# Performance work log

Hardware: AMD Instinct MI355X
Metric: run time of the kernel (lower is better)

Reference implementation:

```python
import jax, jax.numpy as jnp
import numpy as np

K = 8            # regular-rep dim (C_8), reg_dim
R_BINS = 3       # num_radii
T_BINS = 16      # num_theta
G = R_BINS * T_BINS
RADIUS = 40.0    # radius_scale
DT = 1.0
CORR = 1.0 / 128.0
SHIFT = 0.2
TWO_PI = 2.0 * np.pi

# [m,n] -> (m-n) mod K, for circulant (group-equivariant) linear maps on the regular rep
_SIDX = (np.arange(K)[:, None] - np.arange(K)[None, :]) % K


def _basis(ab):
    # learnable equivariant intertwiner rho1 <-> regular: a*u_m + b*u_m_perp
    th = jnp.arange(K, dtype=jnp.float32) * (TWO_PI / K)
    U = jnp.stack([jnp.cos(th), jnp.sin(th)], -1)       # [K,2]
    Up = jnp.stack([-jnp.sin(th), jnp.cos(th)], -1)
    return ab[0] * U + ab[1] * Up


def lift_rho1_to_reg(v, ab):
    # v [...,c,2] -> [...,c,K]
    return jnp.einsum('...ca,ma->...cm', v, _basis(ab))


def proj_reg_to_rho1(x, ab):
    # x [...,c,K] -> [...,c,2]
    return jnp.einsum('...cm,ma->...ca', x, _basis(ab))


def equi_linear_reg(x, W):
    # x [...,ci,K], W [co,ci,K]; out[...,o,m] = sum_{i,s} W[o,i,s] x[...,i,(m-s)%K]
    Wc = W[:, :, _SIDX]                                  # [co,ci,m,n]
    return jnp.einsum('...in,oimn->...om', x, Wc)


def _full_kernel(W):
    # base W [co,ci,K,R,T] -> rotated stack [K(m),co,ci,K(n),G]
    s = T_BINS // K
    kern = jnp.stack([jnp.roll(jnp.roll(W, m, axis=2), m * s, axis=4) for m in range(K)], 0)
    return kern.reshape(K, W.shape[0], W.shape[1], K, G)


def pair_bin_weights(p, mask):
    # Dense pairwise continuous-conv weights: window * bilinear polar-grid interpolation,
    # normalized by the neighbor window sum. p [B,N,2], mask [B,N] -> [B,N,N,G]
    N = p.shape[1]
    rel = p[:, None, :, :] - p[:, :, None, :]            # rel[b,i,j] = p_j - p_i
    d = jnp.sqrt(jnp.sum(rel * rel, -1) + 1e-12) / RADIUS
    window = jnp.maximum(1.0 - d * d, 0.0) ** 3          # radius cutoff + window
    wb = window * mask[:, None, :]
    wb = wb / (jnp.sum(wb, -1, keepdims=True) + 1e-6)    # neighbor normalization
    rc = jnp.clip(d * R_BINS - 0.5, 0.0, R_BINS - 1.0)
    r0 = jnp.floor(rc); wr = rc - r0
    r0i = r0.astype(jnp.int32); r1i = jnp.minimum(r0i + 1, R_BINS - 1)
    eye = jnp.eye(N, dtype=bool)[None]                   # safe atan2 at self-pairs
    rx = jnp.where(eye, 1.0, rel[..., 0]); ry = jnp.where(eye, 0.0, rel[..., 1])
    tc = (jnp.arctan2(ry, rx) % TWO_PI) / TWO_PI * T_BINS
    t0 = jnp.floor(tc); wt = tc - t0
    t0i = t0.astype(jnp.int32) % T_BINS; t1i = (t0i + 1) % T_BINS
    gs = [r0i * T_BINS + t0i, r0i * T_BINS + t1i, r1i * T_BINS + t0i, r1i * T_BINS + t1i]
    ws = [(1 - wr) * (1 - wt), (1 - wr) * wt, wr * (1 - wt), wr * wt]
    Wsum = jnp.zeros(d.shape + (G,), jnp.float32)
    for g, w in zip(gs, ws):
        Wsum = Wsum + (w * wb)[..., None] * jax.nn.one_hot(g, G, dtype=jnp.float32)
    return Wsum


def cts_conv(Wsum, feats, Wk):
    # feats [B,N,ci,K] -> [B,N,co,K]
    F = jnp.einsum('bijg,bjcn->bigcn', Wsum, feats)      # bin neighbor features onto polar grid
    return jnp.einsum('bigcn,mocng->biom', F, _full_kernel(Wk))


def mag_act(x):
    mags = jnp.sum(x * x, -1, keepdims=True) + 1e-6
    return x / mags * jax.nn.relu(mags - SHIFT)


def setup_inputs() -> dict:
    key = jax.random.key(0)
    B, N, T = 2, 512, 7
    ks = jax.random.split(key, 20)
    s = 0.05
    return {
        'p0_enc': jax.random.uniform(ks[0], (B, N, T, 2), jnp.float32) * 100.0,
        'v0_enc': jax.random.normal(ks[1], (B, N, T, 2), jnp.float32),
        'p0': jax.random.uniform(ks[2], (B, N, 2), jnp.float32) * 100.0,
        'v0': jax.random.normal(ks[3], (B, N, 2), jnp.float32),
        'a': jax.random.normal(ks[4], (B, N, 2), jnp.float32) * 0.1,
        'fluid_mask': jnp.ones((B, N), jnp.float32),
        'lift_c0': jax.random.normal(ks[5], (2,), jnp.float32) * s,
        'Wc0': jax.random.normal(ks[6], (4, 16, K, R_BINS, T_BINS), jnp.float32) * s,
        'lift_d0': jax.random.normal(ks[7], (2,), jnp.float32) * s,
        'Wd0': jax.random.normal(ks[8], (4, 16, K), jnp.float32) * s,
        'Wc1': jax.random.normal(ks[9], (8, 8, K, R_BINS, T_BINS), jnp.float32) * s,
        'Wd1': jax.random.normal(ks[10], (8, 8, K), jnp.float32) * s,
        'Wc2': jax.random.normal(ks[11], (16, 8, K, R_BINS, T_BINS), jnp.float32) * s,
        'Wd2': jax.random.normal(ks[12], (16, 8, K), jnp.float32) * s,
        'Wc3': jax.random.normal(ks[13], (8, 16, K, R_BINS, T_BINS), jnp.float32) * s,
        'Wd3': jax.random.normal(ks[14], (8, 16, K), jnp.float32) * s,
        'Wc4': jax.random.normal(ks[15], (3, 8, K, R_BINS, T_BINS), jnp.float32) * s,
        'proj_c4': jax.random.normal(ks[16], (2,), jnp.float32) * s,
        'Wd4': jax.random.normal(ks[17], (3, 8, K), jnp.float32) * s,
        'proj_d4': jax.random.normal(ks[18], (2,), jnp.float32) * s,
    }


def reference(p0_enc, v0_enc, p0, v0, a, fluid_mask,
              lift_c0, Wc0, lift_d0, Wd0, Wc1, Wd1, Wc2, Wd2,
              Wc3, Wd3, Wc4, proj_c4, Wd4, proj_d4):
    feats = jnp.concatenate([v0_enc, p0_enc], -2)        # [B,N,14,2]
    v1 = v0 + DT * a
    p1 = p0 + DT * (v0 + v1) / 2.0
    fluid_feats = jnp.concatenate([v1[:, :, None, :], p1[:, :, None, :], feats], -2)  # [B,N,16,2]
    Wsum = pair_bin_weights(p1, fluid_mask)              # shared across all conv layers
    out_conv = cts_conv(Wsum, lift_rho1_to_reg(fluid_feats, lift_c0), Wc0)
    out_dense = equi_linear_reg(lift_rho1_to_reg(fluid_feats, lift_d0), Wd0)
    output = jnp.concatenate([out_conv, out_dense], -2)  # [B,N,8,K]
    for Wc, Wd, last in ((Wc1, Wd1, False), (Wc2, Wd2, False), (Wc3, Wd3, False), (Wc4, Wd4, True)):
        in_feats = mag_act(output)
        oc = cts_conv(Wsum, in_feats, Wc)
        od = equi_linear_reg(in_feats, Wd)
        if last:
            oc = proj_reg_to_rho1(oc, proj_c4)
            od = proj_reg_to_rho1(od, proj_d4)
        new = oc + od
        if new.shape[-2] == output.shape[-2] and new.shape[-1] == output.shape[-1]:
            new = new + output
        output = new
    pos_correction = CORR * output                       # [B,N,3,2]
    p_corr = p1 + pos_correction[..., 0, :]
    v_corr = (p_corr - p0) / DT
    m_matrix = pos_correction[..., 1:, :]                # [B,N,2,2]
    return p_corr, v_corr, m_matrix
```

## Files before the change

### kernel.cpp

```cpp
#include <hip/hip_runtime.h>

#define NPART 1024
#define NNB   512
#define EMAX  2048

__global__ void prep_kernel(const float* __restrict__ p0_enc, const float* __restrict__ v0_enc,
                            const float* __restrict__ p0, const float* __restrict__ v0,
                            const float* __restrict__ a, const float* __restrict__ liftc,
                            const float* __restrict__ liftd,
                            float* __restrict__ featsC, float* __restrict__ Fbuf,
                            float* __restrict__ p1out)
{
    int p = blockIdx.x;
    int t = threadIdx.x;
    int c = t >> 3, m = t & 7;
    float v0x = v0[p*2+0], v0y = v0[p*2+1];
    float ax  = a[p*2+0],  ay  = a[p*2+1];
    float p0x = p0[p*2+0], p0y = p0[p*2+1];
    float v1x = v0x + ax, v1y = v0y + ay;
    float p1x = p0x + 0.5f*(v0x + v1x), p1y = p0y + 0.5f*(v0y + v1y);
    float vx, vy;
    if (c == 0)      { vx = v1x; vy = v1y; }
    else if (c == 1) { vx = p1x; vy = p1y; }
    else if (c < 9)  { vx = v0_enc[(p*7 + (c-2))*2+0]; vy = v0_enc[(p*7 + (c-2))*2+1]; }
    else             { vx = p0_enc[(p*7 + (c-9))*2+0]; vy = p0_enc[(p*7 + (c-9))*2+1]; }
    float th = (float)m * 0.7853981633974483f;
    float cs = cosf(th), sn = sinf(th);
    float lc0 = liftc[0], lc1 = liftc[1];
    float ld0 = liftd[0], ld1 = liftd[1];
    featsC[p*128 + t]        = vx*(lc0*cs - lc1*sn) + vy*(lc0*sn + lc1*cs);
    Fbuf[p*6272 + 6144 + t]  = vx*(ld0*cs - ld1*sn) + vy*(ld0*sn + ld1*cs);
    if (t == 0) { p1out[p*2+0] = p1x; p1out[p*2+1] = p1y; }
}

__global__ void pairs_kernel(const float* __restrict__ p1, const float* __restrict__ mask,
                             float* __restrict__ Ew, unsigned short* __restrict__ Ej,
                             int* __restrict__ offG)
{
    int p  = blockIdx.x;
    int b  = p >> 9;
    int ii = p & 511;
    int tid = threadIdx.x;
    __shared__ float red[256];
    __shared__ float denomS;
    __shared__ int bincnt[48];
    __shared__ int binoff[49];
    __shared__ int binpos[48];
    if (tid < 48) bincnt[tid] = 0;
    float pix = p1[p*2+0], piy = p1[p*2+1];
    float relx[2], rely[2], dd[2], ww[2];
#pragma unroll
    for (int q = 0; q < 2; ++q) {
        int j  = tid + q*256;
        int jr = b*NNB + j;
        float rx = p1[jr*2+0] - pix;
        float ry = p1[jr*2+1] - piy;
        float d  = sqrtf(rx*rx + ry*ry + 1e-12f) * (1.0f/40.0f);
        float t1 = fmaxf(1.0f - d*d, 0.0f);
        float w  = t1*t1*t1 * mask[jr];
        relx[q] = rx; rely[q] = ry; dd[q] = d; ww[q] = w;
    }
    red[tid] = ww[0] + ww[1];
    __syncthreads();
    for (int s = 128; s > 0; s >>= 1) {
        if (tid < s) red[tid] += red[tid+s];
        __syncthreads();
    }
    if (tid == 0) denomS = 1.0f / (red[0] + 1e-6f);
    __syncthreads();
    float dinv = denomS;

    float wsub[2][4];
    int   bsub[2][4];
#pragma unroll
    for (int q = 0; q < 2; ++q) {
        int j  = tid + q*256;
        if (ww[q] == 0.0f) {
#pragma unroll
            for (int k = 0; k < 4; ++k) wsub[q][k] = 0.0f;
            continue;
        }
        float wb = ww[q] * dinv;
        float d  = dd[q];
        float rc  = fminf(fmaxf(d*3.0f - 0.5f, 0.0f), 2.0f);
        float r0f = floorf(rc);
        float wr  = rc - r0f;
        int r0 = (int)r0f;
        int r1 = min(r0 + 1, 2);
        float rx = (j == ii) ? 1.0f : relx[q];
        float ry = (j == ii) ? 0.0f : rely[q];
        float ang = atan2f(ry, rx);
        if (ang < 0.0f) ang += 6.283185307179586f;
        float tc  = ang * 2.546479089470325f;
        float t0f = floorf(tc);
        float wt  = tc - t0f;
        int t0  = ((int)t0f) & 15;
        int t1i = (t0 + 1) & 15;
        wsub[q][0] = wb * (1.0f-wr) * (1.0f-wt);  bsub[q][0] = r0*16 + t0;
        wsub[q][1] = wb * (1.0f-wr) * wt;         bsub[q][1] = r0*16 + t1i;
        wsub[q][2] = wb * wr * (1.0f-wt);         bsub[q][2] = r1*16 + t0;
        wsub[q][3] = wb * wr * wt;                bsub[q][3] = r1*16 + t1i;
#pragma unroll
        for (int k = 0; k < 4; ++k)
            if (wsub[q][k] != 0.0f) atomicAdd(&bincnt[bsub[q][k]], 1);
    }
    __syncthreads();
    if (tid == 0) {
        int s = 0;
#pragma unroll
        for (int g = 0; g < 48; ++g) { binoff[g] = s; s += bincnt[g]; }
        binoff[48] = s;
    }
    __syncthreads();
    if (tid < 48) binpos[tid] = binoff[tid];
    if (tid < 49) offG[p*64 + tid] = binoff[tid];
    __syncthreads();
#pragma unroll
    for (int q = 0; q < 2; ++q) {
        int j = tid + q*256;
#pragma unroll
        for (int k = 0; k < 4; ++k) {
            if (wsub[q][k] != 0.0f) {
                int slot = atomicAdd(&binpos[bsub[q][k]], 1);
                Ew[p*EMAX + slot] = wsub[q][k];
                Ej[p*EMAX + slot] = (unsigned short)j;
            }
        }
    }
}

#define LMQ(B, W0,W1,W2,W3, J0,J1,J2,J3) do {                                              \
    int _b = (B);                                                                          \
    { int _q=_b+0; bool _v=_q<len; float2 _m=ebuf[_v? e0+_q : e0]; W0=_v?_m.x:0.0f; J0=(int)__float_as_uint(_m.y); } \
    { int _q=_b+1; bool _v=_q<len; float2 _m=ebuf[_v? e0+_q : e0]; W1=_v?_m.x:0.0f; J1=(int)__float_as_uint(_m.y); } \
    { int _q=_b+2; bool _v=_q<len; float2 _m=ebuf[_v? e0+_q : e0]; W2=_v?_m.x:0.0f; J2=(int)__float_as_uint(_m.y); } \
    { int _q=_b+3; bool _v=_q<len; float2 _m=ebuf[_v? e0+_q : e0]; W3=_v?_m.x:0.0f; J3=(int)__float_as_uint(_m.y); } \
} while(0)

template<int PT>
__global__ __launch_bounds__(512) void aggregate_kernel(const float* __restrict__ actsrc, int actStride,
                                                        int C8,
                                                        const float* __restrict__ Ew,
                                                        const unsigned short* __restrict__ Ej,
                                                        const int* __restrict__ offG,
                                                        float* __restrict__ Fbuf, int Krow)
{
    __shared__ float  rows[512*64];
    __shared__ float2 ebuf[EMAX];
    __shared__ int    soff[49];
    int tid  = threadIdx.x;
    int lane = tid & 63;
    int wv   = tid >> 6;
    int choff = blockIdx.y * 64;
    int p0   = blockIdx.x * PT;
    int pbase = p0 & ~511;

    {
        float4* r4 = (float4*)rows;
#pragma unroll
        for (int k = 0; k < 16; ++k) {
            int idx4 = tid + k*512;
            int r = idx4 >> 4, c = (idx4 & 15) * 4;
            r4[idx4] = *(const float4*)(actsrc + (size_t)(pbase + r)*actStride + choff + c);
        }
    }

    for (int pp = 0; pp < PT; ++pp) {
        int p = p0 + pp;
        __syncthreads();
        if (tid < 49) soff[tid] = offG[p*64 + tid];
        __syncthreads();
        int cnt = soff[48];
        for (int i = tid; i < cnt; i += 512) {
            float2 e; e.x = Ew[p*EMAX + i]; e.y = __uint_as_float((unsigned)Ej[p*EMAX + i]);
            ebuf[i] = e;
        }
        __syncthreads();

        float* dst = Fbuf + (size_t)p * Krow + choff + lane;
#pragma unroll
        for (int s = 0; s < 6; ++s) {
            int g = wv + s*8;
            int e0 = soff[g], e1 = soff[g+1];
            int len = e1 - e0;
            float a0 = 0.0f, a1 = 0.0f, a2 = 0.0f, a3 = 0.0f;
            if (len > 0) {
                int nq = (len + 3) >> 2;
                float wa0,wa1,wa2,wa3, wb0,wb1,wb2,wb3;
                int   ja0,ja1,ja2,ja3, jb0,jb1,jb2,jb3;
                LMQ(0, wa0,wa1,wa2,wa3, ja0,ja1,ja2,ja3);
                float fa0 = rows[ja0*64 + lane];
                float fa1 = rows[ja1*64 + lane];
                float fa2 = rows[ja2*64 + lane];
                float fa3 = rows[ja3*64 + lane];
                LMQ(4, wb0,wb1,wb2,wb3, jb0,jb1,jb2,jb3);
                for (int iq = 0; iq < nq; ++iq) {
                    float wc0,wc1,wc2,wc3; int jc0,jc1,jc2,jc3;
                    LMQ((iq+2)*4, wc0,wc1,wc2,wc3, jc0,jc1,jc2,jc3);
                    float fb0 = rows[jb0*64 + lane];
                    float fb1 = rows[jb1*64 + lane];
                    float fb2 = rows[jb2*64 + lane];
                    float fb3 = rows[jb3*64 + lane];
                    a0 = fmaf(wa0, fa0, a0);
                    a1 = fmaf(wa1, fa1, a1);
                    a2 = fmaf(wa2, fa2, a2);
                    a3 = fmaf(wa3, fa3, a3);
                    wa0=wb0; wa1=wb1; wa2=wb2; wa3=wb3;
                    fa0=fb0; fa1=fb1; fa2=fb2; fa3=fb3;
                    wb0=wc0; wb1=wc1; wb2=wc2; wb3=wc3;
                    jb0=jc0; jb1=jc1; jb2=jc2; jb3=jc3;
                }
            }
            dst[g*C8] = (a0 + a1) + (a2 + a3);
        }
    }
}

__global__ void expand_kernel(const float* __restrict__ Wc, const float* __restrict__ Wd,
                              const float* __restrict__ pc4, const float* __restrict__ pd4,
                              float* __restrict__ Bm, int C, int O8, int total, int mode)
{
    int e = blockIdx.x*blockDim.x + threadIdx.x;
    if (e >= total) return;
    int col = e % O8;
    int k   = e / O8;
    int C8  = C*8;
    bool conv = (k < 48*C8);
    int cc, nn, rr = 0, tt = 0;
    if (conv) {
        int g = k / C8, rem = k - g*C8;
        cc = rem >> 3; nn = rem & 7; rr = g >> 4; tt = g & 15;
    } else {
        int rem = k - 48*C8;
        cc = rem >> 3; nn = rem & 7;
    }
    float val = 0.0f;
    if (mode == 0) {
        int o = col >> 3, m = col & 7;
        if (conv) val = Wc[(((o*C + cc)*8 + ((nn - m) & 7))*3 + rr)*16 + ((tt - 2*m) & 15)];
        else      val = Wd[(o*C + cc)*8 + ((m - nn) & 7)];
    } else if (mode == 1) {
        int o = col >> 3, m = col & 7;
        if (col < 32) { if (conv)  val = Wc[(((o*C + cc)*8 + ((nn - m)&7))*3 + rr)*16 + ((tt - 2*m)&15)]; }
        else          { if (!conv) val = Wd[((o-4)*C + cc)*8 + ((m - nn)&7)]; }
    } else {
        if (col < 6) {
            int co = col >> 1, aa = col & 1;
            float s0 = conv ? pc4[0] : pd4[0];
            float s1 = conv ? pc4[1] : pd4[1];
#pragma unroll
            for (int m = 0; m < 8; ++m) {
                float th = (float)m * 0.7853981633974483f;
                float csv = cosf(th), snv = sinf(th);
                float bas = (aa == 0) ? (s0*csv - s1*snv) : (s0*snv + s1*csv);
                float wv;
                if (conv) wv = Wc[(((co*C + cc)*8 + ((nn - m)&7))*3 + rr)*16 + ((tt - 2*m)&15)];
                else      wv = Wd[(co*C + cc)*8 + ((m - nn)&7)];
                val += wv * bas;
            }
        }
    }
    Bm[e] = val;
}

template<int N>
__global__ __launch_bounds__(256) void gemm_tile(const float* __restrict__ A, int Kdim,
                                                 const float* __restrict__ B,
                                                 float* __restrict__ Cpart)
{
    constexpr int CT = N/16;
    __shared__ float As[32][68];
    __shared__ float Bs[32][N];
    int tid = threadIdx.x;
    int tr = tid & 15, tc = tid >> 4;
    int m0 = blockIdx.x * 64;
    int k0base = blockIdx.y * 224;
    float acc[4][CT];
#pragma unroll
    for (int i = 0; i < 4; ++i)
#pragma unroll
        for (int u = 0; u < CT; ++u) acc[i][u] = 0.0f;

    int ar = tid >> 2, aq = (tid & 3) * 8;
    for (int k0 = 0; k0 < 224; k0 += 32) {
        const float* Ap = A + (size_t)(m0 + ar)*Kdim + k0base + k0 + aq;
        float4 av0 = *(const float4*)(Ap);
        float4 av1 = *(const float4*)(Ap + 4);
        As[aq+0][ar] = av0.x; As[aq+1][ar] = av0.y; As[aq+2][ar] = av0.z; As[aq+3][ar] = av0.w;
        As[aq+4][ar] = av1.x; As[aq+5][ar] = av1.y; As[aq+6][ar] = av1.z; As[aq+7][ar] = av1.w;
#pragma unroll
        for (int u = 0; u < (8*N + 255)/256; ++u) {
            int idx = tid + 256*u;
            if (idx < 8*N) {
                int row = idx / (N/4), c4 = idx % (N/4);
                *(float4*)&Bs[row][c4*4] = *(const float4*)(B + (size_t)(k0base + k0 + row)*N + c4*4);
            }
        }
        __syncthreads();
#pragma unroll
        for (int kk = 0; kk < 32; ++kk) {
            float4 a4 = *(const float4*)&As[kk][tr*4];
            if (CT == 1) {
                float bv = Bs[kk][tc];
                acc[0][0] += a4.x*bv; acc[1][0] += a4.y*bv;
                acc[2][0] += a4.z*bv; acc[3][0] += a4.w*bv;
            } else {
#pragma unroll
                for (int uu = 0; uu < CT; uu += 4) {
                    float4 b4 = *(const float4*)&Bs[kk][tc*CT + uu];
                    acc[0][uu+0] += a4.x*b4.x; acc[0][uu+1] += a4.x*b4.y; acc[0][uu+2] += a4.x*b4.z; acc[0][uu+3] += a4.x*b4.w;
                    acc[1][uu+0] += a4.y*b4.x; acc[1][uu+1] += a4.y*b4.y; acc[1][uu+2] += a4.y*b4.z; acc[1][uu+3] += a4.y*b4.w;
                    acc[2][uu+0] += a4.z*b4.x; acc[2][uu+1] += a4.z*b4.y; acc[2][uu+2] += a4.z*b4.z; acc[2][uu+3] += a4.z*b4.w;
                    acc[3][uu+0] += a4.w*b4.x; acc[3][uu+1] += a4.w*b4.y; acc[3][uu+2] += a4.w*b4.z; acc[3][uu+3] += a4.w*b4.w;
                }
            }
        }
        __syncthreads();
    }
    float* Cp = Cpart + ((size_t)blockIdx.y*1024 + m0)*N;
#pragma unroll
    for (int i = 0; i < 4; ++i)
#pragma unroll
        for (int u = 0; u < CT; ++u)
            Cp[(size_t)(tr*4 + i)*N + tc*CT + u] = acc[i][u];
}

__global__ void epilogue_kernel(const float* __restrict__ Cpart, int S, int O, int res,
                                float* __restrict__ outBuf, float* __restrict__ actDst, int actStride)
{
    int id = blockIdx.x*blockDim.x + threadIdx.x;
    if (id >= NPART*O) return;
    int p = id / O, c = id % O;
    int O8 = O*8;
    float x[8];
#pragma unroll
    for (int m = 0; m < 8; ++m) x[m] = 0.0f;
    for (int s = 0; s < S; ++s) {
        const float4* q = (const float4*)(Cpart + ((size_t)(s*1024 + p))*O8 + c*8);
        float4 u0 = q[0], u1 = q[1];
        x[0]+=u0.x; x[1]+=u0.y; x[2]+=u0.z; x[3]+=u0.w;
        x[4]+=u1.x; x[5]+=u1.y; x[6]+=u1.z; x[7]+=u1.w;
    }
    float* ob = outBuf + (size_t)p*O8 + c*8;
    float mag = 1e-6f;
#pragma unroll
    for (int m = 0; m < 8; ++m) {
        float v = x[m];
        if (res) v += ob[m];
        x[m] = v; mag += v*v;
    }
#pragma unroll
    for (int m = 0; m < 8; ++m) ob[m] = x[m];
    float sc = fmaxf(mag - 0.2f, 0.0f) / mag;
    float* ad = actDst + (size_t)p*actStride + c*8;
#pragma unroll
    for (int m = 0; m < 8; ++m) ad[m] = x[m]*sc;
}

__global__ void final_kernel(const float* __restrict__ Cpart, int S, const float* __restrict__ p1,
                             const float* __restrict__ p0, float* __restrict__ out)
{
    int p = blockIdx.x*blockDim.x + threadIdx.x;
    if (p >= NPART) return;
    float c[6];
#pragma unroll
    for (int t = 0; t < 6; ++t) c[t] = 0.0f;
    for (int s = 0; s < S; ++s) {
        const float* q = Cpart + ((size_t)(s*1024 + p))*16;
#pragma unroll
        for (int t = 0; t < 6; ++t) c[t] += q[t];
    }
    const float sc = 0.0078125f;
#pragma unroll
    for (int t = 0; t < 6; ++t) c[t] *= sc;
    float pcx = p1[p*2+0] + c[0], pcy = p1[p*2+1] + c[1];
    out[p*2+0] = pcx; out[p*2+1] = pcy;
    out[2048 + p*2+0] = pcx - p0[p*2+0];
    out[2048 + p*2+1] = pcy - p0[p*2+1];
    out[4096 + p*4+0] = c[2]; out[4096 + p*4+1] = c[3];
    out[4096 + p*4+2] = c[4]; out[4096 + p*4+3] = c[5];
}

extern "C" void kernel_launch(void* const* d_in, const int* in_sizes, int n_in,
                              void* d_out, int out_size, void* d_ws, size_t ws_size,
                              hipStream_t stream)
{
    const float* p0_enc  = (const float*)d_in[0];
    const float* v0_enc  = (const float*)d_in[1];
    const float* p0      = (const float*)d_in[2];
    const float* v0      = (const float*)d_in[3];
    const float* a       = (const float*)d_in[4];
    const float* mask    = (const float*)d_in[5];
    const float* lift_c0 = (const float*)d_in[6];
    const float* Wc0     = (const float*)d_in[7];
    const float* lift_d0 = (const float*)d_in[8];
    const float* Wd0     = (const float*)d_in[9];
    const float* Wc1     = (const float*)d_in[10];
    const float* Wd1     = (const float*)d_in[11];
    const float* Wc2     = (const float*)d_in[12];
    const float* Wd2     = (const float*)d_in[13];
    const float* Wc3     = (const float*)d_in[14];
    const float* Wd3     = (const float*)d_in[15];
    const float* Wc4     = (const float*)d_in[16];
    const float* pc4     = (const float*)d_in[17];
    const float* Wd4     = (const float*)d_in[18];
    const float* pd4     = (const float*)d_in[19];
    float* out = (float*)d_out;

    float* wsf    = (float*)d_ws;
    float* featsC = wsf;
    float* p1     = featsC + 131072;
    float* Ew     = p1 + 2048;
    unsigned short* Ej = (unsigned short*)(Ew + 2097152);
    int*   offG   = (int*)(Ew + 2097152 + 1048576);
    float* Fbuf   = (float*)offG + 65536;
    float* Cpart  = Fbuf + 1024*6272;
    float* outBuf = Cpart + 1835008;
    float* Bm0    = outBuf + 131072;
    float* Bm1    = Bm0 + 6272*64;
    float* Bm2    = Bm1 + 3136*64;
    float* Bm3    = Bm2 + 3136*128;
    float* Bm4    = Bm3 + 6272*64;

    prep_kernel<<<NPART, 128, 0, stream>>>(p0_enc, v0_enc, p0, v0, a, lift_c0, lift_d0,
                                           featsC, Fbuf, p1);
    pairs_kernel<<<NPART, 256, 0, stream>>>(p1, mask, Ew, Ej, offG);

    {
        int t0 = 6272*64;  expand_kernel<<<(t0+255)/256, 256, 0, stream>>>(Wc0, Wd0, pc4, pd4, Bm0, 16,  64, t0, 1);
        int t1 = 3136*64;  expand_kernel<<<(t1+255)/256, 256, 0, stream>>>(Wc1, Wd1, pc4, pd4, Bm1,  8,  64, t1, 0);
        int t2 = 3136*128; expand_kernel<<<(t2+255)/256, 256, 0, stream>>>(Wc2, Wd2, pc4, pd4, Bm2,  8, 128, t2, 0);
        int t3 = 6272*64;  expand_kernel<<<(t3+255)/256, 256, 0, stream>>>(Wc3, Wd3, pc4, pd4, Bm3, 16,  64, t3, 0);
        int t4 = 3136*16;  expand_kernel<<<(t4+255)/256, 256, 0, stream>>>(Wc4, Wd4, pc4, pd4, Bm4,  8,  16, t4, 2);
    }

    aggregate_kernel<8><<<dim3(128,2), 512, 0, stream>>>(featsC, 128, 128, Ew, Ej, offG, Fbuf, 6272);
    gemm_tile<64><<<dim3(16,28), 256, 0, stream>>>(Fbuf, 6272, Bm0, Cpart);
    epilogue_kernel<<<(NPART*8+63)/64, 64, 0, stream>>>(Cpart, 28, 8, 0, outBuf, Fbuf + 3072, 3136);
    aggregate_kernel<4><<<dim3(256,1), 512, 0, stream>>>(Fbuf + 3072, 3136, 64, Ew, Ej, offG, Fbuf, 3136);
    gemm_tile<64><<<dim3(16,14), 256, 0, stream>>>(Fbuf, 3136, Bm1, Cpart);
    epilogue_kernel<<<(NPART*8+63)/64, 64, 0, stream>>>(Cpart, 14, 8, 1, outBuf, Fbuf + 3072, 3136);
    aggregate_kernel<4><<<dim3(256,1), 512, 0, stream>>>(Fbuf + 3072, 3136, 64, Ew, Ej, offG, Fbuf, 3136);
    gemm_tile<128><<<dim3(16,14), 256, 0, stream>>>(Fbuf, 3136, Bm2, Cpart);
    epilogue_kernel<<<(NPART*16+63)/64, 64, 0, stream>>>(Cpart, 14, 16, 0, outBuf, Fbuf + 6144, 6272);
    aggregate_kernel<8><<<dim3(128,2), 512, 0, stream>>>(Fbuf + 6144, 6272, 128, Ew, Ej, offG, Fbuf, 6272);
    gemm_tile<64><<<dim3(16,28), 256, 0, stream>>>(Fbuf, 6272, Bm3, Cpart);
    epilogue_kernel<<<(NPART*8+63)/64, 64, 0, stream>>>(Cpart, 28, 8, 0, outBuf, Fbuf + 3072, 3136);
    aggregate_kernel<4><<<dim3(256,1), 512, 0, stream>>>(Fbuf + 3072, 3136, 64, Ew, Ej, offG, Fbuf, 3136);
    gemm_tile<16><<<dim3(16,14), 256, 0, stream>>>(Fbuf, 3136, Bm4, Cpart);
    final_kernel<<<4, 256, 0, stream>>>(Cpart, 14, p1, p0, out);
}
```

Before: 457.4 us.

## Vectorize aggregate gather with float4 LDS rows split across lane groups

The neighbor aggregation loop now has each wavefront split into four lane groups. Each group handles a different edge of every quad, and each lane reads a float4 of four channels from shared memory instead of one scalar. The shared row buffer is padded to a stride of 68 floats so the strided float4 reads avoid bank conflicts. Partial sums are combined with cross-lane xor shuffles and written out as one float4 per lane. The aim is to cut the number of LDS instructions and broadcast edge loads per edge. In exchange it adds shuffle reductions, a larger shared-memory footprint, and more idle lanes on short bins.

```diff
diff --git a/kernel.cpp b/kernel.cpp
--- a/kernel.cpp
+++ b/kernel.cpp
@@ -129,14 +129,6 @@
     }
 }
 
-#define LMQ(B, W0,W1,W2,W3, J0,J1,J2,J3) do {                                              \
-    int _b = (B);                                                                          \
-    { int _q=_b+0; bool _v=_q<len; float2 _m=ebuf[_v? e0+_q : e0]; W0=_v?_m.x:0.0f; J0=(int)__float_as_uint(_m.y); } \
-    { int _q=_b+1; bool _v=_q<len; float2 _m=ebuf[_v? e0+_q : e0]; W1=_v?_m.x:0.0f; J1=(int)__float_as_uint(_m.y); } \
-    { int _q=_b+2; bool _v=_q<len; float2 _m=ebuf[_v? e0+_q : e0]; W2=_v?_m.x:0.0f; J2=(int)__float_as_uint(_m.y); } \
-    { int _q=_b+3; bool _v=_q<len; float2 _m=ebuf[_v? e0+_q : e0]; W3=_v?_m.x:0.0f; J3=(int)__float_as_uint(_m.y); } \
-} while(0)
-
 template<int PT>
 __global__ __launch_bounds__(512) void aggregate_kernel(const float* __restrict__ actsrc, int actStride,
                                                         int C8,
@@ -145,12 +137,14 @@
                                                         const int* __restrict__ offG,
                                                         float* __restrict__ Fbuf, int Krow)
 {
-    __shared__ float  rows[512*64];
+    __shared__ float  rows[512*68];
     __shared__ float2 ebuf[EMAX];
     __shared__ int    soff[49];
     int tid  = threadIdx.x;
     int lane = tid & 63;
     int wv   = tid >> 6;
+    int slot = lane >> 4;
+    int c4   = lane & 15;
     int choff = blockIdx.y * 64;
     int p0   = blockIdx.x * PT;
     int pbase = p0 & ~511;
@@ -160,10 +154,11 @@
 #pragma unroll
         for (int k = 0; k < 16; ++k) {
             int idx4 = tid + k*512;
-            int r = idx4 >> 4, c = (idx4 & 15) * 4;
-            r4[idx4] = *(const float4*)(actsrc + (size_t)(pbase + r)*actStride + choff + c);
-        }
-    }
+            int r = idx4 >> 4, q = idx4 & 15;
+            r4[r*17 + q] = *(const float4*)(actsrc + (size_t)(pbase + r)*actStride + choff + q*4);
+        }
+    }
+    const float4* rowf4 = (const float4*)rows;
 
     for (int pp = 0; pp < PT; ++pp) {
         int p = p0 + pp;
@@ -177,41 +172,50 @@
         }
         __syncthreads();
 
-        float* dst = Fbuf + (size_t)p * Krow + choff + lane;
+        float* dst = Fbuf + (size_t)p * Krow + choff;
 #pragma unroll
         for (int s = 0; s < 6; ++s) {
             int g = wv + s*8;
             int e0 = soff[g], e1 = soff[g+1];
             int len = e1 - e0;
-            float a0 = 0.0f, a1 = 0.0f, a2 = 0.0f, a3 = 0.0f;
+            float4 acc = make_float4(0.f, 0.f, 0.f, 0.f);
             if (len > 0) {
                 int nq = (len + 3) >> 2;
-                float wa0,wa1,wa2,wa3, wb0,wb1,wb2,wb3;
-                int   ja0,ja1,ja2,ja3, jb0,jb1,jb2,jb3;
-                LMQ(0, wa0,wa1,wa2,wa3, ja0,ja1,ja2,ja3);
-                float fa0 = rows[ja0*64 + lane];
-                float fa1 = rows[ja1*64 + lane];
-                float fa2 = rows[ja2*64 + lane];
-                float fa3 = rows[ja3*64 + lane];
-                LMQ(4, wb0,wb1,wb2,wb3, jb0,jb1,jb2,jb3);
+                float wA, wB; float4 fA, fB;
+                {
+                    int qo = slot; bool v = qo < len; int em = v ? (e0 + qo) : e0;
+                    float2 m = ebuf[em];
+                    wA = v ? m.x : 0.0f;
+                    int j = (int)__float_as_uint(m.y);
+                    fA = rowf4[j*17 + c4];
+                }
+                {
+                    int qo = 4 + slot; bool v = qo < len; int em = v ? (e0 + qo) : e0;
+                    float2 m = ebuf[em];
+                    wB = v ? m.x : 0.0f;
+                    int j = (int)__float_as_uint(m.y);
+                    fB = rowf4[j*17 + c4];
+                }
                 for (int iq = 0; iq < nq; ++iq) {
-                    float wc0,wc1,wc2,wc3; int jc0,jc1,jc2,jc3;
-                    LMQ((iq+2)*4, wc0,wc1,wc2,wc3, jc0,jc1,jc2,jc3);
-                    float fb0 = rows[jb0*64 + lane];
-                    float fb1 = rows[jb1*64 + lane];
-                    float fb2 = rows[jb2*64 + lane];
-                    float fb3 = rows[jb3*64 + lane];
-                    a0 = fmaf(wa0, fa0, a0);
-                    a1 = fmaf(wa1, fa1, a1);
-                    a2 = fmaf(wa2, fa2, a2);
-                    a3 = fmaf(wa3, fa3, a3);
-                    wa0=wb0; wa1=wb1; wa2=wb2; wa3=wb3;
-                    fa0=fb0; fa1=fb1; fa2=fb2; fa3=fb3;
-                    wb0=wc0; wb1=wc1; wb2=wc2; wb3=wc3;
-                    jb0=jc0; jb1=jc1; jb2=jc2; jb3=jc3;
+                    float4 f = fA; float w = wA;
+                    fA = fB; wA = wB;
+                    int qo = (iq + 2)*4 + slot;
+                    bool v = qo < len; int em = v ? (e0 + qo) : e0;
+                    float2 m = ebuf[em];
+                    wB = v ? m.x : 0.0f;
+                    int j = (int)__float_as_uint(m.y);
+                    fB = rowf4[j*17 + c4];
+                    acc.x = fmaf(w, f.x, acc.x);
+                    acc.y = fmaf(w, f.y, acc.y);
+                    acc.z = fmaf(w, f.z, acc.z);
+                    acc.w = fmaf(w, f.w, acc.w);
                 }
             }
-            dst[g*C8] = (a0 + a1) + (a2 + a3);
+            acc.x += __shfl_xor(acc.x, 16, 64); acc.x += __shfl_xor(acc.x, 32, 64);
+            acc.y += __shfl_xor(acc.y, 16, 64); acc.y += __shfl_xor(acc.y, 32, 64);
+            acc.z += __shfl_xor(acc.z, 16, 64); acc.z += __shfl_xor(acc.z, 32, 64);
+            acc.w += __shfl_xor(acc.w, 16, 64); acc.w += __shfl_xor(acc.w, 32, 64);
+            if (slot == 0) *(float4*)(dst + g*C8 + c4*4) = acc;
         }
     }
 }
```

Result: faster. 395.5 us (-13.5%).
